# Optimization experiments

Measured on AMD Instinct MI355X. Metric: run time of the kernel, lower is better.

Reference implementation:

```python
import jax, jax.numpy as jnp
import numpy as np
import math

D_QKV = 64


def setup_inputs() -> dict:
    key = jax.random.key(0)
    ks = jax.random.split(key, 6)
    b, l, d_model, n_head, d_qkv = 2, 2048, 1024, 16, D_QKV
    return {
        "x": jax.random.normal(ks[0], (b, l, d_model), dtype=jnp.float32),
        "w_q": jax.random.normal(ks[1], (n_head, d_model, d_qkv), dtype=jnp.float32) * (2.0 / (d_model + d_qkv)) ** 0.5,
        "w_k": jax.random.normal(ks[2], (n_head, d_model, d_qkv), dtype=jnp.float32) * (2.0 / (d_model + d_qkv)) ** 0.5,
        "w_v": jax.random.normal(ks[3], (n_head, d_model, d_qkv), dtype=jnp.float32) * (2.0 / (d_model + d_qkv)) ** 0.5,
        "w_o": jax.random.normal(ks[4], (n_head, d_qkv, d_model), dtype=jnp.float32) * (2.0 / (d_model + d_qkv)) ** 0.5,
        "mask": jnp.zeros((b, 1, 1, l), dtype=bool),  # True = masked (padding)
    }


def reference(x, w_q, w_k, w_v, w_o, mask):
    # x: [b, l, m]; w_{q,k,v}: [n, m, d]; w_o: [n, d, m]; mask broadcastable to [b, n, l, l]
    q = jnp.einsum("blm,nmd->bnld", x, w_q)
    k = jnp.einsum("blm,nmd->bnld", x, w_k)
    v = jnp.einsum("blm,nmd->bnld", x, w_v)
    scores = jnp.einsum("bnld,bnkd->bnlk", q, k) / math.sqrt(D_QKV)
    scores = jnp.where(mask, jnp.float32(-1e9), scores)
    attn = jax.nn.softmax(scores, axis=-1)  # dropout is identity (p=0 / eval)
    ctx = jnp.einsum("bnlk,bnkd->bnld", attn, v)
    # per-head output projection then sum over heads: V.matmul(w_o).sum(dim=1)
    return jnp.einsum("bnld,ndm->blm", ctx, w_o)
```

## Files before the change

kernel.cpp:

```cpp
#include <hip/hip_runtime.h>
#include <stdint.h>

using bf16x8  = __attribute__((ext_vector_type(8))) short;
using f32x4   = __attribute__((ext_vector_type(4))) float;
using f32x16  = __attribute__((ext_vector_type(16))) float;
using ushort8 = __attribute__((ext_vector_type(8))) unsigned short;
using ushort4v= __attribute__((ext_vector_type(4))) unsigned short;
using uint2v  = __attribute__((ext_vector_type(2))) unsigned int;

typedef __attribute__((address_space(1))) const unsigned int* gas_ptr;
typedef __attribute__((address_space(3))) unsigned int*       las_ptr;

__device__ __forceinline__ void gload_lds16(const unsigned short* g, unsigned short* l) {
    __builtin_amdgcn_global_load_lds((gas_ptr)(const void*)g, (las_ptr)(void*)l, 16, 0, 0);
}

__device__ __forceinline__ unsigned short f2bf(float f) {
    union { float f; uint32_t u; } x; x.f = f;
    uint32_t u = x.u;
    uint32_t r = u + 0x7fffu + ((u >> 16) & 1u);
    return (unsigned short)(r >> 16);
}
__device__ __forceinline__ float bf2f(unsigned short u) {
    union { uint32_t u; float f; } x; x.u = ((uint32_t)u) << 16;
    return x.f;
}

__device__ __forceinline__ f32x4 mfma16(bf16x8 a, bf16x8 b, f32x4 c) {
    return __builtin_amdgcn_mfma_f32_16x16x32_bf16(a, b, c, 0, 0, 0);
}
__device__ __forceinline__ f32x16 mfma32(bf16x8 a, bf16x8 b, f32x16 c) {
    return __builtin_amdgcn_mfma_f32_32x32x16_bf16(a, b, c, 0, 0, 0);
}

__device__ __forceinline__ unsigned int cvtpk_bf16(float lo, float hi) {
    unsigned int r;
    asm("v_cvt_pk_bf16_f32 %0, %1, %2" : "=v"(r) : "v"(lo), "v"(hi));
    return r;
}
__device__ __forceinline__ void plswap(unsigned int& a, unsigned int& b) {
    asm("v_permlane32_swap_b32 %0, %1" : "+v"(a), "+v"(b));
}
__device__ __forceinline__ float m3(float a, float b, float c) {
    return fmaxf(fmaxf(a, b), c);
}


__global__ void cast_x_kernel(const float* __restrict__ x, unsigned short* __restrict__ xb) {
    int i = blockIdx.x * 256 + threadIdx.x;
    using f32x4v = __attribute__((ext_vector_type(4))) float;
    f32x4v v = ((const f32x4v*)x)[i];
    ushort4v o;
    o[0] = f2bf(v[0]); o[1] = f2bf(v[1]); o[2] = f2bf(v[2]); o[3] = f2bf(v[3]);
    ((ushort4v*)xb)[i] = o;
}

__global__ void pack_wqkv_t(const float* __restrict__ wq, const float* __restrict__ wk,
                            const float* __restrict__ wv, unsigned short* __restrict__ wpT) {
    __shared__ float tile[64][65];
    const int mm = blockIdx.y;
    const int s = mm >> 4, hh = mm & 15;
    const float* src = ((s == 0) ? wq : (s == 1) ? wk : wv) + (size_t)hh * 1024 * 64;
    const int k0 = blockIdx.x * 64;
    const int c = threadIdx.x & 63, rg = threadIdx.x >> 6;
#pragma unroll
    for (int i = 0; i < 16; ++i) {
        int r = rg * 16 + i;
        tile[r][c] = src[(size_t)(k0 + r) * 64 + c];
    }
    __syncthreads();
    unsigned short* dst = wpT + ((size_t)s * 1024 + hh * 64) * 1024 + k0;
    const int kc = threadIdx.x & 63, dg = threadIdx.x >> 6;
#pragma unroll
    for (int i = 0; i < 16; ++i) {
        int d = dg * 16 + i;
        dst[(size_t)d * 1024 + kc] = f2bf(tile[kc][d]);
    }
}

__global__ void pack_wo_t(const float* __restrict__ wo, unsigned short* __restrict__ woT) {
    __shared__ float tile[64][65];
    const int r0 = blockIdx.y * 64;
    const int c0 = blockIdx.x * 64;
    const int c = threadIdx.x & 63, rg = threadIdx.x >> 6;
#pragma unroll
    for (int i = 0; i < 16; ++i) {
        int r = rg * 16 + i;
        tile[r][c] = wo[(size_t)(r0 + r) * 1024 + c0 + c];
    }
    __syncthreads();
    const int kc = threadIdx.x & 63, mg = threadIdx.x >> 6;
#pragma unroll
    for (int i = 0; i < 16; ++i) {
        int m = mg * 16 + i;
        woT[(size_t)(c0 + m) * 1024 + r0 + kc] = f2bf(tile[kc][m]);
    }
}


template<int MODE, int BN>
__global__ __launch_bounds__(256) void gemm_bt(
    const unsigned short* __restrict__ A,
    const unsigned short* __restrict__ BT,
    float* __restrict__ Cf,
    unsigned short* __restrict__ Q,
    unsigned short* __restrict__ Kq,
    unsigned short* __restrict__ V,
    int M, int N, int K)
{
    constexpr int NF = BN / 32;
    __shared__ unsigned short As[128 * 64];
    __shared__ unsigned short Bs[BN * 64];
    const int tid  = threadIdx.x;
    const int lane = tid & 63;
    const int wave = tid >> 6;
    const int wm = wave >> 1, wn = wave & 1;
    const int l15 = lane & 15, l4 = lane >> 4;
    const int row0 = blockIdx.y * 128;
    const int col0 = blockIdx.x * BN;

    f32x4 acc[4][NF];
#pragma unroll
    for (int i = 0; i < 4; ++i)
#pragma unroll
        for (int j = 0; j < NF; ++j) acc[i][j] = (f32x4){0.f, 0.f, 0.f, 0.f};

    for (int k0 = 0; k0 < K; k0 += 64) {
        __syncthreads();
#pragma unroll
        for (int it = 0; it < 4; ++it) {
            int cb = (it * 4 + wave) * 64;
            int c  = cb + lane;
            int r  = c >> 3, c8 = c & 7;
            int sc8 = c8 ^ (r & 7);
            gload_lds16(&A[(size_t)(row0 + r) * K + k0 + sc8 * 8], &As[cb * 8]);
        }
#pragma unroll
        for (int it = 0; it < NF; ++it) {
            int cb = (it * 4 + wave) * 64;
            int c  = cb + lane;
            int r  = c >> 3, c8 = c & 7;
            int sc8 = c8 ^ (r & 7);
            gload_lds16(&BT[(size_t)(col0 + r) * K + k0 + sc8 * 8], &Bs[cb * 8]);
        }
        __syncthreads();
#pragma unroll
        for (int kk = 0; kk < 2; ++kk) {
            bf16x8 af[4], bfr[NF];
#pragma unroll
            for (int m = 0; m < 4; ++m) {
                int r   = wm * 64 + m * 16 + l15;
                int blk = (kk * 4 + l4) ^ (r & 7);
                af[m] = *(const bf16x8*)&As[r * 64 + blk * 8];
            }
#pragma unroll
            for (int n = 0; n < NF; ++n) {
                int r   = wn * (BN / 2) + n * 16 + l15;
                int blk = (kk * 4 + l4) ^ (r & 7);
                bfr[n] = *(const bf16x8*)&Bs[r * 64 + blk * 8];
            }
#pragma unroll
            for (int m = 0; m < 4; ++m)
#pragma unroll
                for (int n = 0; n < NF; ++n)
                    acc[m][n] = mfma16(af[m], bfr[n], acc[m][n]);
        }
    }

#pragma unroll
    for (int m = 0; m < 4; ++m) {
        int gr0 = row0 + wm * 64 + m * 16 + l4 * 4;
#pragma unroll
        for (int n = 0; n < NF; ++n) {
            int gc = col0 + wn * (BN / 2) + n * 16 + l15;
            if (MODE == 0) {
                int s = gc >> 10, rem = gc & 1023;
                int hh = rem >> 6, dd = rem & 63;
                int bb = gr0 >> 11, ll = gr0 & 2047;
                if (s == 2) {
                    ushort4v o;
#pragma unroll
                    for (int r = 0; r < 4; ++r) o[r] = f2bf(acc[m][n][r]);
                    *(ushort4v*)&V[(((size_t)bb * 16 + hh) * 64 + dd) * 2048 + ll] = o;
                } else {
                    unsigned short* dst = (s == 0) ? Q : Kq;
#pragma unroll
                    for (int r = 0; r < 4; ++r)
                        dst[(((size_t)bb * 16 + hh) * 2048 + ll + r) * 64 + dd] = f2bf(acc[m][n][r]);
                }
            } else {
#pragma unroll
                for (int r = 0; r < 4; ++r)
                    Cf[(size_t)(gr0 + r) * N + gc] = acc[m][n][r];
            }
        }
    }
}


__global__ __launch_bounds__(256, 4) void attn_kernel(
    const unsigned short* __restrict__ qb,
    const unsigned short* __restrict__ kb,
    const unsigned short* __restrict__ vtb,
    const unsigned char* __restrict__ mask,
    unsigned short* __restrict__ part0,
    unsigned short* __restrict__ part1,
    float* __restrict__ ml)
{
    const int lg = blockIdx.x;
    int u = ((lg & 7) << 7) | (lg >> 3);
    int bh = u >> 5, sub = u & 31;
    const int qt = sub >> 1, half = sub & 1;
    const int b = bh >> 4;
    const int t0 = half * 16;
    const int NT = 16;

    const int tid  = threadIdx.x;
    const int lane = tid & 63, wave = tid >> 6;
    const int l31  = lane & 31, hi = lane >> 5;

    __shared__ unsigned short smem[16384];
    __shared__ int flags[32];

    const size_t hoff = (size_t)bh * 131072;
    const unsigned short* qh  = qb  + hoff;
    const unsigned short* kh  = kb  + hoff;
    const unsigned short* vth = vtb + hoff;
    const unsigned char*  mb  = mask + (size_t)b * 2048;

    if (tid < 32) flags[tid] = 0;
    __syncthreads();
    {
        uint2v mv = *(const uint2v*)&mb[tid * 8];
        if (mv[0] | mv[1]) flags[tid >> 3] = 1;
    }

    const int qrow = qt * 128 + wave * 32 + l31;
    bf16x8 qf[4];
#pragma unroll
    for (int ki = 0; ki < 4; ++ki)
        qf[ki] = *(const bf16x8*)&qh[(size_t)qrow * 64 + ki * 16 + hi * 8];

    const f32x16 zf = {0,0,0,0,0,0,0,0,0,0,0,0,0,0,0,0};
    bf16x8 ones;
#pragma unroll
    for (int j = 0; j < 8; ++j) ones[j] = (short)0x3F80;

    f32x16 accA = {0,0,0,0,0,0,0,0,0,0,0,0,0,0,0,0};
    f32x16 accB = {0,0,0,0,0,0,0,0,0,0,0,0,0,0,0,0};
    f32x16 accL = {0,0,0,0,0,0,0,0,0,0,0,0,0,0,0,0};
    float m_r = -1e30f;
    const float SC  = 0.18033688011112042f;
    const float THR = 44.3614195558365f;

#define STAGE(KB, VB, KV0) do {                                                          \
        _Pragma("unroll")                                                                \
        for (int it_ = 0; it_ < 2; ++it_) {                                              \
            int c_ = it_ * 256 + tid;                                                    \
            int r_ = c_ >> 3, c8_ = c_ & 7;                                              \
            int sc8_ = c8_ ^ (r_ & 7);                                                   \
            gload_lds16(&kh[(size_t)((KV0) + r_) * 64 + sc8_ * 8],                       \
                        &(KB)[(it_ * 256 + wave * 64) * 8]);                             \
            gload_lds16(&vth[(size_t)r_ * 2048 + (KV0) + sc8_ * 8],                      \
                        &(VB)[(it_ * 256 + wave * 64) * 8]);                             \
        }                                                                                \
    } while (0)

    STAGE(smem, smem + 8192, t0 * 64);

    for (int t = t0; t < t0 + NT; ++t) {
        const int kv0 = t * 64;
        unsigned short* Kb = smem + ((t - t0) & 1) * 4096;
        unsigned short* Vb = smem + 8192 + ((t - t0) & 1) * 4096;
        __syncthreads();
        if (t + 1 < t0 + NT) {
            unsigned short* Kn = smem + ((t + 1 - t0) & 1) * 4096;
            unsigned short* Vn = smem + 8192 + ((t + 1 - t0) & 1) * 4096;
            STAGE(Kn, Vn, kv0 + 64);
        }

        f32x16 s0, s1;
        __builtin_amdgcn_s_setprio(1);
        {
            int c0 = (hi ^ (l31 & 7)) * 8;
            bf16x8 a0 = *(const bf16x8*)&Kb[l31 * 64 + c0];
            bf16x8 a1 = *(const bf16x8*)&Kb[(32 + l31) * 64 + c0];
            s0 = mfma32(a0, qf[0], zf);
            s1 = mfma32(a1, qf[0], zf);
        }
#pragma unroll
        for (int ki = 1; ki < 4; ++ki) {
            int c0 = ((ki * 2 + hi) ^ (l31 & 7)) * 8;
            bf16x8 a0 = *(const bf16x8*)&Kb[l31 * 64 + c0];
            bf16x8 a1 = *(const bf16x8*)&Kb[(32 + l31) * 64 + c0];
            s0 = mfma32(a0, qf[ki], s0);
            s1 = mfma32(a1, qf[ki], s1);
        }
        __builtin_amdgcn_s_setprio(0);

        if (flags[t]) {
#pragma unroll
            for (int r = 0; r < 16; ++r) {
                int keyl = (r & 3) + 8 * (r >> 2) + 4 * hi;
                if (mb[kv0 + keyl])      s0[r] = -1e30f;
                if (mb[kv0 + 32 + keyl]) s1[r] = -1e30f;
            }
        }

        float mx;
        {
            float a0 = m3(s0[0],  s0[1],  s0[2]);
            float a1 = m3(s0[3],  s0[4],  s0[5]);
            float a2 = m3(s0[6],  s0[7],  s0[8]);
            float a3 = m3(s0[9],  s0[10], s0[11]);
            float a4 = m3(s0[12], s0[13], s0[14]);
            float b0 = m3(s1[0],  s1[1],  s1[2]);
            float b1 = m3(s1[3],  s1[4],  s1[5]);
            float b2 = m3(s1[6],  s1[7],  s1[8]);
            float b3 = m3(s1[9],  s1[10], s1[11]);
            float b4 = m3(s1[12], s1[13], s1[14]);
            float c0 = m3(a0, a1, s0[15]);
            float c1 = m3(a2, a3, a4);
            float c2 = m3(b0, b1, s1[15]);
            float c3 = m3(b2, b3, b4);
            mx = fmaxf(m3(c0, c1, c2), c3);
        }
        mx = fmaxf(mx, __shfl_xor(mx, 32));
        if (__any(mx > m_r + THR)) {
            float mn  = fmaxf(m_r, mx);
            float scl = __builtin_amdgcn_exp2f((m_r - mn) * SC);
            m_r = mn;
            accL[0] *= scl;
#pragma unroll
            for (int i = 0; i < 16; ++i) { accA[i] *= scl; accB[i] *= scl; }
        }
        const float nmc = -m_r * SC;
#pragma unroll
        for (int i = 0; i < 16; ++i) {
            s0[i] = __builtin_amdgcn_exp2f(__builtin_fmaf(s0[i], SC, nmc));
            s1[i] = __builtin_amdgcn_exp2f(__builtin_fmaf(s1[i], SC, nmc));
        }

        bf16x8 pf[4];
        {
            union { unsigned int u[4]; bf16x8 v; } f;
            unsigned int w0 = cvtpk_bf16(s0[0],  s0[1]),  w1 = cvtpk_bf16(s0[2],  s0[3]);
            unsigned int w2 = cvtpk_bf16(s0[4],  s0[5]),  w3 = cvtpk_bf16(s0[6],  s0[7]);
            unsigned int w4 = cvtpk_bf16(s0[8],  s0[9]),  w5 = cvtpk_bf16(s0[10], s0[11]);
            unsigned int w6 = cvtpk_bf16(s0[12], s0[13]), w7 = cvtpk_bf16(s0[14], s0[15]);
            plswap(w0, w2); plswap(w1, w3); plswap(w4, w6); plswap(w5, w7);
            f.u[0] = w0; f.u[1] = w1; f.u[2] = w2; f.u[3] = w3; pf[0] = f.v;
            f.u[0] = w4; f.u[1] = w5; f.u[2] = w6; f.u[3] = w7; pf[1] = f.v;
            unsigned int x0 = cvtpk_bf16(s1[0],  s1[1]),  x1 = cvtpk_bf16(s1[2],  s1[3]);
            unsigned int x2 = cvtpk_bf16(s1[4],  s1[5]),  x3 = cvtpk_bf16(s1[6],  s1[7]);
            unsigned int x4 = cvtpk_bf16(s1[8],  s1[9]),  x5 = cvtpk_bf16(s1[10], s1[11]);
            unsigned int x6 = cvtpk_bf16(s1[12], s1[13]), x7 = cvtpk_bf16(s1[14], s1[15]);
            plswap(x0, x2); plswap(x1, x3); plswap(x4, x6); plswap(x5, x7);
            f.u[0] = x0; f.u[1] = x1; f.u[2] = x2; f.u[3] = x3; pf[2] = f.v;
            f.u[0] = x4; f.u[1] = x5; f.u[2] = x6; f.u[3] = x7; pf[3] = f.v;
        }

        __builtin_amdgcn_s_setprio(1);
#pragma unroll
        for (int ks = 0; ks < 4; ++ks) {
            int c0 = ((ks * 2 + hi) ^ (l31 & 7)) * 8;
            bf16x8 vA = *(const bf16x8*)&Vb[l31 * 64 + c0];
            bf16x8 vB = *(const bf16x8*)&Vb[(32 + l31) * 64 + c0];
            accA = mfma32(vA, pf[ks], accA);
            accB = mfma32(vB, pf[ks], accB);
            accL = mfma32(ones, pf[ks], accL);
        }
        __builtin_amdgcn_s_setprio(0);
    }
#undef STAGE

    __syncthreads();
    const int qloc = wave * 32 + l31;
#pragma unroll
    for (int r = 0; r < 16; ++r) {
        int dA = (r & 3) + 8 * (r >> 2) + 4 * hi;
        smem[qloc * 64 + (dA ^ ((qloc & 7) * 8))]        = f2bf(accA[r]);
        smem[qloc * 64 + ((32 + dA) ^ ((qloc & 7) * 8))] = f2bf(accB[r]);
    }
    if (hi == 0) {
        size_t mrow = ((size_t)half * 32 + bh) * 2048 + qt * 128 + qloc;
        *(float2*)&ml[mrow * 2] = make_float2(m_r, accL[0]);
    }
    __syncthreads();
    unsigned short* pdst = half ? part1 : part0;
    const size_t prow0 = (size_t)bh * 2048 + qt * 128;
#pragma unroll
    for (int it = 0; it < 4; ++it) {
        int idx = tid + it * 256;
        int q = idx >> 3, c = idx & 7;
        ushort8 vv = *(const ushort8*)&smem[q * 64 + ((c * 8) ^ ((q & 7) * 8))];
        *(ushort8*)&pdst[(prow0 + q) * 64 + c * 8] = vv;
    }
}


__global__ void combine_kernel(const unsigned short* __restrict__ part0,
                               const unsigned short* __restrict__ part1,
                               const float* __restrict__ ml,
                               unsigned short* __restrict__ ctxb)
{
    const float SC = 0.18033688011112042f;
    int gid = blockIdx.x * 256 + threadIdx.x;
    int row = gid >> 3, c = gid & 7;
    ushort8 v0 = *(const ushort8*)&part0[(size_t)row * 64 + c * 8];
    ushort8 v1 = *(const ushort8*)&part1[(size_t)row * 64 + c * 8];
    float2 a = *(const float2*)&ml[(size_t)row * 2];
    float2 d = *(const float2*)&ml[(size_t)(65536 + row) * 2];
    float m  = fmaxf(a.x, d.x);
    float w0 = __builtin_amdgcn_exp2f((a.x - m) * SC);
    float w1 = __builtin_amdgcn_exp2f((d.x - m) * SC);
    float li = 1.0f / (a.y * w0 + d.y * w1);
    ushort8 o;
#pragma unroll
    for (int j = 0; j < 8; ++j)
        o[j] = f2bf((bf2f(v0[j]) * w0 + bf2f(v1[j]) * w1) * li);
    int bh = row >> 11, ql = row & 2047;
    int bb = bh >> 4, hh = bh & 15;
    *(ushort8*)&ctxb[((size_t)(bb * 2048 + ql)) * 1024 + hh * 64 + c * 8] = o;
}


extern "C" void kernel_launch(void* const* d_in, const int* in_sizes, int n_in,
                              void* d_out, int out_size, void* d_ws, size_t ws_size,
                              hipStream_t stream)
{
    const float* x  = (const float*)d_in[0];
    const float* wq = (const float*)d_in[1];
    const float* wk = (const float*)d_in[2];
    const float* wv = (const float*)d_in[3];
    const float* wo = (const float*)d_in[4];
    const unsigned char* mask = (const unsigned char*)d_in[5];
    float* out = (float*)d_out;

    char* ws = (char*)d_ws;
    unsigned short* xb   = (unsigned short*)(ws);
    unsigned short* wpT  = (unsigned short*)(ws + 8388608);
    unsigned short* woT  = (unsigned short*)(ws + 14680064);
    unsigned short* qb   = (unsigned short*)(ws + 16777216);
    unsigned short* kb   = (unsigned short*)(ws + 25165824);
    unsigned short* vtb  = (unsigned short*)(ws + 33554432);
    unsigned short* ctxb = (unsigned short*)(ws + 41943040);
    unsigned short* part0 = (unsigned short*)d_out;
    unsigned short* part1 = (unsigned short*)d_out + 4194304;
    float*          mlb   = (float*)wpT;

    cast_x_kernel<<<4096, 256, 0, stream>>>(x, xb);
    pack_wqkv_t  <<<dim3(16, 48), 256, 0, stream>>>(wq, wk, wv, wpT);
    pack_wo_t    <<<dim3(16, 16), 256, 0, stream>>>(wo, woT);

    gemm_bt<0,128><<<dim3(24, 32), 256, 0, stream>>>(xb, wpT, nullptr, qb, kb, vtb, 4096, 3072, 1024);

    attn_kernel<<<1024, 256, 0, stream>>>(qb, kb, vtb, mask, part0, part1, mlb);
    combine_kernel<<<2048, 256, 0, stream>>>(part0, part1, mlb, ctxb);

    gemm_bt<1,64><<<dim3(16, 32), 256, 0, stream>>>(ctxb, woT, out, nullptr, nullptr, nullptr, 4096, 1024, 1024);
}
```

Baseline: 128.3 us.

## Split attention KV range three ways and single-buffer V tiles to cut LDS

Raises the split-KV factor of the attention kernel from two to three (11/11/10 tiles), launching 1536 blocks instead of 1024 and adding a third partial buffer plus a three-way merge in the combine kernel. V staging drops to a single buffer that is loaded after each iteration's compute, which shrinks LDS from 32KB to 24KB, and launch bounds rise to 6 blocks per SIMD for higher occupancy. The aim is better CU utilisation and latency hiding. The cost is that V loads are no longer prefetched, so they are exposed behind an extra barrier, and the combine kernel does more memory traffic. The third partial buffer reuses the cast-x workspace, which is dead after the QKV GEMM.

Result: slower. 360.2 us (+180.8%).

```diff
diff --git a/kernel.cpp b/kernel.cpp
--- a/kernel.cpp
+++ b/kernel.cpp
@@ -198,28 +198,31 @@
 }
 
 
-__global__ __launch_bounds__(256, 4) void attn_kernel(
+__global__ __launch_bounds__(256, 6) void attn_kernel(
     const unsigned short* __restrict__ qb,
     const unsigned short* __restrict__ kb,
     const unsigned short* __restrict__ vtb,
     const unsigned char* __restrict__ mask,
     unsigned short* __restrict__ part0,
     unsigned short* __restrict__ part1,
+    unsigned short* __restrict__ part2,
     float* __restrict__ ml)
 {
     const int lg = blockIdx.x;
-    int u = ((lg & 7) << 7) | (lg >> 3);
-    int bh = u >> 5, sub = u & 31;
-    const int qt = sub >> 1, half = sub & 1;
+    int u = (lg & 7) * 192 + (lg >> 3);
+    const int bh = u / 48;
+    int rem = u - bh * 48;
+    const int qt = rem / 3;
+    const int sp = rem - qt * 3;
     const int b = bh >> 4;
-    const int t0 = half * 16;
-    const int NT = 16;
+    const int t0 = sp * 11;
+    const int NT = (sp == 2) ? 10 : 11;
 
     const int tid  = threadIdx.x;
     const int lane = tid & 63, wave = tid >> 6;
     const int l31  = lane & 31, hi = lane >> 5;
 
-    __shared__ unsigned short smem[16384];
+    __shared__ unsigned short smem[12288];
     __shared__ int flags[32];
 
     const size_t hoff = (size_t)bh * 131072;
@@ -253,7 +256,7 @@
     const float SC  = 0.18033688011112042f;
     const float THR = 44.3614195558365f;
 
-#define STAGE(KB, VB, KV0) do {                                                          \
+#define STAGE_K(KB, KV0) do {                                                            \
         _Pragma("unroll")                                                                \
         for (int it_ = 0; it_ < 2; ++it_) {                                              \
             int c_ = it_ * 256 + tid;                                                    \
@@ -261,23 +264,31 @@
             int sc8_ = c8_ ^ (r_ & 7);                                                   \
             gload_lds16(&kh[(size_t)((KV0) + r_) * 64 + sc8_ * 8],                       \
                         &(KB)[(it_ * 256 + wave * 64) * 8]);                             \
+        }                                                                                \
+    } while (0)
+#define STAGE_V(VB, KV0) do {                                                            \
+        _Pragma("unroll")                                                                \
+        for (int it_ = 0; it_ < 2; ++it_) {                                              \
+            int c_ = it_ * 256 + tid;                                                    \
+            int r_ = c_ >> 3, c8_ = c_ & 7;                                              \
+            int sc8_ = c8_ ^ (r_ & 7);                                                   \
             gload_lds16(&vth[(size_t)r_ * 2048 + (KV0) + sc8_ * 8],                      \
                         &(VB)[(it_ * 256 + wave * 64) * 8]);                             \
         }                                                                                \
     } while (0)
 
-    STAGE(smem, smem + 8192, t0 * 64);
-
-    for (int t = t0; t < t0 + NT; ++t) {
+    STAGE_K(smem, t0 * 64);
+    STAGE_V(smem + 8192, t0 * 64);
+
+    int par = 0;
+    for (int i = 0; i < NT; ++i) {
+        const int t   = t0 + i;
         const int kv0 = t * 64;
-        unsigned short* Kb = smem + ((t - t0) & 1) * 4096;
-        unsigned short* Vb = smem + 8192 + ((t - t0) & 1) * 4096;
+        const unsigned short* Kb = smem + par * 4096;
+        unsigned short*       Vb = smem + 8192;
+
         __syncthreads();
-        if (t + 1 < t0 + NT) {
-            unsigned short* Kn = smem + ((t + 1 - t0) & 1) * 4096;
-            unsigned short* Vn = smem + 8192 + ((t + 1 - t0) & 1) * 4096;
-            STAGE(Kn, Vn, kv0 + 64);
-        }
+        if (i + 1 < NT) STAGE_K(smem + (par ^ 1) * 4096, (t + 1) * 64);
 
         f32x16 s0, s1;
         __builtin_amdgcn_s_setprio(1);
@@ -332,13 +343,13 @@
             m_r = mn;
             accL[0] *= scl;
 #pragma unroll
-            for (int i = 0; i < 16; ++i) { accA[i] *= scl; accB[i] *= scl; }
+            for (int i2 = 0; i2 < 16; ++i2) { accA[i2] *= scl; accB[i2] *= scl; }
         }
         const float nmc = -m_r * SC;
 #pragma unroll
-        for (int i = 0; i < 16; ++i) {
-            s0[i] = __builtin_amdgcn_exp2f(__builtin_fmaf(s0[i], SC, nmc));
-            s1[i] = __builtin_amdgcn_exp2f(__builtin_fmaf(s1[i], SC, nmc));
+        for (int i2 = 0; i2 < 16; ++i2) {
+            s0[i2] = __builtin_amdgcn_exp2f(__builtin_fmaf(s0[i2], SC, nmc));
+            s1[i2] = __builtin_amdgcn_exp2f(__builtin_fmaf(s1[i2], SC, nmc));
         }
 
         bf16x8 pf[4];
@@ -371,10 +382,14 @@
             accL = mfma32(ones, pf[ks], accL);
         }
         __builtin_amdgcn_s_setprio(0);
-    }
-#undef STAGE
-
-    __syncthreads();
+
+        __syncthreads();
+        if (i + 1 < NT) STAGE_V(Vb, (t + 1) * 64);
+        par ^= 1;
+    }
+#undef STAGE_K
+#undef STAGE_V
+
     const int qloc = wave * 32 + l31;
 #pragma unroll
     for (int r = 0; r < 16; ++r) {
@@ -383,11 +398,11 @@
         smem[qloc * 64 + ((32 + dA) ^ ((qloc & 7) * 8))] = f2bf(accB[r]);
     }
     if (hi == 0) {
-        size_t mrow = ((size_t)half * 32 + bh) * 2048 + qt * 128 + qloc;
+        size_t mrow = ((size_t)sp * 32 + bh) * 2048 + qt * 128 + qloc;
         *(float2*)&ml[mrow * 2] = make_float2(m_r, accL[0]);
     }
     __syncthreads();
-    unsigned short* pdst = half ? part1 : part0;
+    unsigned short* pdst = (sp == 0) ? part0 : (sp == 1) ? part1 : part2;
     const size_t prow0 = (size_t)bh * 2048 + qt * 128;
 #pragma unroll
     for (int it = 0; it < 4; ++it) {
@@ -401,6 +416,7 @@
 
 __global__ void combine_kernel(const unsigned short* __restrict__ part0,
                                const unsigned short* __restrict__ part1,
+                               const unsigned short* __restrict__ part2,
                                const float* __restrict__ ml,
                                unsigned short* __restrict__ ctxb)
 {
@@ -409,16 +425,19 @@
     int row = gid >> 3, c = gid & 7;
     ushort8 v0 = *(const ushort8*)&part0[(size_t)row * 64 + c * 8];
     ushort8 v1 = *(const ushort8*)&part1[(size_t)row * 64 + c * 8];
+    ushort8 v2 = *(const ushort8*)&part2[(size_t)row * 64 + c * 8];
     float2 a = *(const float2*)&ml[(size_t)row * 2];
     float2 d = *(const float2*)&ml[(size_t)(65536 + row) * 2];
-    float m  = fmaxf(a.x, d.x);
+    float2 e = *(const float2*)&ml[(size_t)(131072 + row) * 2];
+    float m  = fmaxf(fmaxf(a.x, d.x), e.x);
     float w0 = __builtin_amdgcn_exp2f((a.x - m) * SC);
     float w1 = __builtin_amdgcn_exp2f((d.x - m) * SC);
-    float li = 1.0f / (a.y * w0 + d.y * w1);
+    float w2 = __builtin_amdgcn_exp2f((e.x - m) * SC);
+    float li = 1.0f / (a.y * w0 + d.y * w1 + e.y * w2);
     ushort8 o;
 #pragma unroll
     for (int j = 0; j < 8; ++j)
-        o[j] = f2bf((bf2f(v0[j]) * w0 + bf2f(v1[j]) * w1) * li);
+        o[j] = f2bf((bf2f(v0[j]) * w0 + bf2f(v1[j]) * w1 + bf2f(v2[j]) * w2) * li);
     int bh = row >> 11, ql = row & 2047;
     int bb = bh >> 4, hh = bh & 15;
     *(ushort8*)&ctxb[((size_t)(bb * 2048 + ql)) * 1024 + hh * 64 + c * 8] = o;
@@ -447,6 +466,7 @@
     unsigned short* ctxb = (unsigned short*)(ws + 41943040);
     unsigned short* part0 = (unsigned short*)d_out;
     unsigned short* part1 = (unsigned short*)d_out + 4194304;
+    unsigned short* part2 = xb;
     float*          mlb   = (float*)wpT;
 
     cast_x_kernel<<<4096, 256, 0, stream>>>(x, xb);
@@ -455,8 +475,8 @@
 
     gemm_bt<0,128><<<dim3(24, 32), 256, 0, stream>>>(xb, wpT, nullptr, qb, kb, vtb, 4096, 3072, 1024);
 
-    attn_kernel<<<1024, 256, 0, stream>>>(qb, kb, vtb, mask, part0, part1, mlb);
-    combine_kernel<<<2048, 256, 0, stream>>>(part0, part1, mlb, ctxb);
+    attn_kernel<<<1536, 256, 0, stream>>>(qb, kb, vtb, mask, part0, part1, part2, mlb);
+    combine_kernel<<<2048, 256, 0, stream>>>(part0, part1, part2, mlb, ctxb);
 
     gemm_bt<1,64><<<dim3(16, 32), 256, 0, stream>>>(ctxb, woT, out, nullptr, nullptr, nullptr, 4096, 1024, 1024);
 }
```
